# Optimization experiments

Measured on AMD Instinct MI355X. Metric: run time of the kernel, lower is better.

The kernel has to match this reference:

```python
import jax, jax.numpy as jnp
import numpy as np

N_EMBD = 1024
N_HEAD = 16
HEAD_DIM = N_EMBD // N_HEAD


def setup_inputs() -> dict:
    key = jax.random.key(0)
    ks = jax.random.split(key, 5)
    B, T, C = 2, 2048, N_EMBD
    scale = 0.02
    return {
        "x": jax.random.normal(ks[0], (B, T, C), dtype=jnp.float32),
        "w_attn": jax.random.normal(ks[1], (C, 3 * C), dtype=jnp.float32) * scale,
        "b_attn": jax.random.normal(ks[2], (3 * C,), dtype=jnp.float32) * scale,
        "w_proj": jax.random.normal(ks[3], (C, C), dtype=jnp.float32) * scale,
        "b_proj": jax.random.normal(ks[4], (C,), dtype=jnp.float32) * scale,
    }


def reference(x, w_attn, b_attn, w_proj, b_proj):
    B, T, C = x.shape
    H, D = N_HEAD, HEAD_DIM
    qkv = x @ w_attn + b_attn  # [B,T,3C]
    q, k, v = jnp.split(qkv, 3, axis=-1)
    # [B,T,C] -> [B,H,T,D]
    q = q.reshape(B, T, H, D).transpose(0, 2, 1, 3)
    k = k.reshape(B, T, H, D).transpose(0, 2, 1, 3)
    v = v.reshape(B, T, H, D).transpose(0, 2, 1, 3)
    scores = jnp.einsum("bhqd,bhkd->bhqk", q, k) / jnp.sqrt(jnp.float32(D))
    causal = jnp.tril(jnp.ones((T, T), dtype=bool))
    scores = jnp.where(causal, scores, jnp.finfo(scores.dtype).min)
    attn = jax.nn.softmax(scores, axis=-1)
    y = jnp.einsum("bhqk,bhkd->bhqd", attn, v)  # [B,H,T,D]
    y = y.transpose(0, 2, 1, 3).reshape(B, T, C)
    return y @ w_proj + b_proj
```

## Files before the change

kernel.cpp:

```cpp
#include <hip/hip_runtime.h>

typedef unsigned short u16;
typedef u16 u16x4 __attribute__((ext_vector_type(4)));
typedef u16 u16x8 __attribute__((ext_vector_type(8)));
typedef __bf16 bf16x8 __attribute__((ext_vector_type(8)));
typedef float floatx4 __attribute__((ext_vector_type(4)));

#define N_EMBD 1024
#define N_HEAD 16
#define HEAD_DIM 64
#define SEQ 2048
#define BATCH 2
#define M_ROWS (BATCH * SEQ)

typedef __attribute__((address_space(1))) const unsigned char ga_t;
typedef __attribute__((address_space(3))) unsigned char la_t;

#if __has_builtin(__builtin_amdgcn_exp2f)
#define EXP2(x) __builtin_amdgcn_exp2f(x)
#else
#define EXP2(x) exp2f(x)
#endif

__device__ __forceinline__ u16 cvt_bf16(float f) {
  return __builtin_bit_cast(u16, (__bf16)f);
}

__global__ __launch_bounds__(256) void prep(const float* __restrict__ x,
                                            u16* __restrict__ xb,
                                            const float* __restrict__ wa,
                                            const float* __restrict__ wp,
                                            u16* __restrict__ outa,
                                            u16* __restrict__ outp) {
  const int bid = blockIdx.x;
  if (bid < 2048) {
    const long i = ((long)bid * 256 + threadIdx.x) * 8;
    const float4 f0 = *(const float4*)&x[i];
    const float4 f1 = *(const float4*)&x[i + 4];
    u16x8 p;
    p[0] = cvt_bf16(f0.x); p[1] = cvt_bf16(f0.y);
    p[2] = cvt_bf16(f0.z); p[3] = cvt_bf16(f0.w);
    p[4] = cvt_bf16(f1.x); p[5] = cvt_bf16(f1.y);
    p[6] = cvt_bf16(f1.z); p[7] = cvt_bf16(f1.w);
    *(u16x8*)&xb[i] = p;
    return;
  }
  __shared__ u16 tile[32][33];
  const int t = bid - 2048;
  const int gx = t & 127;
  const int gy = t >> 7;
  const int R = N_EMBD;
  const float* in;
  u16* out;
  int C, bx;
  if (gx < 96) {
    in = wa; out = outa; C = 3 * N_EMBD; bx = gx * 32;
  } else {
    in = wp; out = outp; C = N_EMBD; bx = (gx - 96) * 32;
  }
  const int by = gy * 32;
  const int tx = threadIdx.x & 31;
  const int ty = threadIdx.x >> 5;
#pragma unroll
  for (int j = 0; j < 32; j += 8)
    tile[ty + j][tx] = cvt_bf16(in[(long)(by + ty + j) * C + bx + tx]);
  __syncthreads();
#pragma unroll
  for (int j = 0; j < 32; j += 8)
    out[(long)(bx + ty + j) * R + by + tx] = tile[tx][ty + j];
}

#define GBK 64

__device__ __forceinline__ void stage192(const u16* __restrict__ A,
                                         const u16* __restrict__ Bt, int bm,
                                         int bn, int kt, int tid, u16* as,
                                         u16* bs) {
#pragma unroll
  for (int i = 0; i < 2; ++i) {
    const int p = tid + 512 * i;
    const int row = p >> 3;
    const int sl = (p & 7) ^ (row & 7);
    const int wb = (i * 512 + (tid & 448)) * 8;
    __builtin_amdgcn_global_load_lds(
        (ga_t*)&A[(long)(bm + row) * N_EMBD + kt + sl * 8], (la_t*)&as[wb], 16,
        0, 0);
  }
#pragma unroll
  for (int i = 0; i < 3; ++i) {
    const int p = tid + 512 * i;
    const int row = p >> 3;
    const int sl = (p & 7) ^ (row & 7);
    const int wb = (i * 512 + (tid & 448)) * 8;
    __builtin_amdgcn_global_load_lds(
        (ga_t*)&Bt[(long)(bn + row) * N_EMBD + kt + sl * 8], (la_t*)&bs[wb], 16,
        0, 0);
  }
}

__global__ __launch_bounds__(512, 4) void gemm_qkv(
    const u16* __restrict__ A, const u16* __restrict__ Bt,
    const float* __restrict__ bias, u16* __restrict__ qo, u16* __restrict__ ko,
    u16* __restrict__ vo) {
  extern __shared__ u16 smem[];
  u16* As = smem;
  u16* Bs = smem + 2 * 128 * 64;
  const int tid = threadIdx.x;

  const int nx = gridDim.x;
  const int nwg = nx * gridDim.y;
  int lin = blockIdx.y * nx + blockIdx.x;
  lin = (lin & 7) * (nwg >> 3) + (lin >> 3);
  const int bm = (lin / nx) * 128;
  const int bn = (lin % nx) * 192;

  const int w = tid >> 6;
  const int l = tid & 63;
  const int wm = (w >> 2) * 64;
  const int wn = (w & 3) * 48;
  const int m16 = l & 15;
  const int quad = l >> 4;
  const int rsw = m16 & 7;

  floatx4 acc[4][3];
#pragma unroll
  for (int i = 0; i < 4; ++i)
#pragma unroll
    for (int j = 0; j < 3; ++j) acc[i][j] = (floatx4){0.f, 0.f, 0.f, 0.f};

  stage192(A, Bt, bm, bn, 0, tid, As, Bs);
  stage192(A, Bt, bm, bn, GBK, tid, As + 128 * 64, Bs + 192 * 64);
  asm volatile("s_waitcnt vmcnt(5)" ::: "memory");
  __builtin_amdgcn_s_barrier();

  for (int kt = 0; kt < 16; ++kt) {
    u16* as = As + (kt & 1) * (128 * 64);
    u16* bs = Bs + (kt & 1) * (192 * 64);

    bf16x8 af[4][2], bf[3][2];
#pragma unroll
    for (int i = 0; i < 4; ++i)
#pragma unroll
      for (int kk = 0; kk < 2; ++kk)
        af[i][kk] = __builtin_bit_cast(
            bf16x8, *(const u16x8*)&as[(wm + i * 16 + m16) * 64 +
                                       (((kk * 4 + quad) ^ rsw) * 8)]);
#pragma unroll
    for (int j = 0; j < 3; ++j)
#pragma unroll
      for (int kk = 0; kk < 2; ++kk)
        bf[j][kk] = __builtin_bit_cast(
            bf16x8, *(const u16x8*)&bs[(wn + j * 16 + m16) * 64 +
                                       (((kk * 4 + quad) ^ rsw) * 8)]);
    asm volatile("s_waitcnt lgkmcnt(0)" ::: "memory");
    __builtin_amdgcn_s_barrier();

    if (kt + 2 < 16) {
      stage192(A, Bt, bm, bn, (kt + 2) * GBK, tid, as, bs);
      asm volatile("s_waitcnt vmcnt(5)" ::: "memory");
    } else {
      asm volatile("s_waitcnt vmcnt(0)" ::: "memory");
    }
    __builtin_amdgcn_s_barrier();

    __builtin_amdgcn_s_setprio(1);
#pragma unroll
    for (int kk = 0; kk < 2; ++kk)
#pragma unroll
      for (int i = 0; i < 4; ++i)
#pragma unroll
        for (int j = 0; j < 3; ++j)
          acc[i][j] = __builtin_amdgcn_mfma_f32_16x16x32_bf16(
              af[i][kk], bf[j][kk], acc[i][j], 0, 0, 0);
    __builtin_amdgcn_s_setprio(0);
  }

#pragma unroll
  for (int i = 0; i < 4; ++i) {
#pragma unroll
    for (int j = 0; j < 3; ++j) {
      const int col = bn + wn + j * 16 + m16;
      const float bv = bias[col];
      const int which = col >> 10;
      const int cc = col & 1023;
      const int h = cc >> 6;
      const int dd = cc & 63;
      const int row0 = bm + wm + i * 16 + quad * 4;
      const int b = row0 >> 11;
      const int t0 = row0 & 2047;
      if (which == 2) {
        u16x4 pk;
#pragma unroll
        for (int r = 0; r < 4; ++r) pk[r] = cvt_bf16(acc[i][j][r] + bv);
        *(u16x4*)&vo[(((long)(b * N_HEAD + h)) * HEAD_DIM + dd) * SEQ + t0] =
            pk;
      } else {
        u16* dst = (which == 0) ? qo : ko;
#pragma unroll
        for (int r = 0; r < 4; ++r)
          dst[(((long)(b * N_HEAD + h)) * SEQ + t0 + r) * HEAD_DIM + dd] =
              cvt_bf16(acc[i][j][r] + bv);
      }
    }
  }
}

#define PBK 64

__device__ __forceinline__ void stage_proj(const u16* __restrict__ A,
                                           const u16* __restrict__ Bt, int bm,
                                           int bn, int kt, int tid, u16* as,
                                           u16* bs) {
  const int head = kt >> 6;
#pragma unroll
  for (int i = 0; i < 4; ++i) {
    const int p = tid + 256 * i;
    const int row = p >> 3;
    const int sl = (p & 7) ^ (row & 7);
    const int wb = (i * 256 + (tid & 192)) * 8;
    const int m = bm + row;
    const int b = m >> 11, t = m & 2047;
    __builtin_amdgcn_global_load_lds(
        (ga_t*)&A[(((long)(b * N_HEAD + head)) * SEQ + t) * HEAD_DIM + sl * 8],
        (la_t*)&as[wb], 16, 0, 0);
  }
#pragma unroll
  for (int i = 0; i < 2; ++i) {
    const int p = tid + 256 * i;
    const int row = p >> 3;
    const int sl = (p & 7) ^ (row & 7);
    const int wb = (i * 256 + (tid & 192)) * 8;
    __builtin_amdgcn_global_load_lds(
        (ga_t*)&Bt[(long)(bn + row) * N_EMBD + kt + sl * 8], (la_t*)&bs[wb], 16,
        0, 0);
  }
}

__global__ __launch_bounds__(256) void gemm_proj(const u16* __restrict__ A,
                                                 const u16* __restrict__ Bt,
                                                 const float* __restrict__ bias,
                                                 float* __restrict__ out) {
  __shared__ u16 As[2][128 * 64];
  __shared__ u16 Bs[2][64 * 64];
  const int tid = threadIdx.x;

  const int nx = gridDim.x;
  const int nwg = nx * gridDim.y;
  int lin = blockIdx.y * nx + blockIdx.x;
  lin = (lin & 7) * (nwg >> 3) + (lin >> 3);
  const int bm = (lin / nx) * 128;
  const int bn = (lin % nx) * 64;

  const int w = tid >> 6;
  const int l = tid & 63;
  const int wm = (w >> 1) * 64;
  const int wn = (w & 1) * 32;
  const int m16 = l & 15;
  const int quad = l >> 4;
  const int rsw = m16 & 7;

  floatx4 acc[4][2];
#pragma unroll
  for (int i = 0; i < 4; ++i)
#pragma unroll
    for (int j = 0; j < 2; ++j) acc[i][j] = (floatx4){0.f, 0.f, 0.f, 0.f};

  stage_proj(A, Bt, bm, bn, 0, tid, As[0], Bs[0]);
  stage_proj(A, Bt, bm, bn, PBK, tid, As[1], Bs[1]);
  asm volatile("s_waitcnt vmcnt(6)" ::: "memory");
  __builtin_amdgcn_s_barrier();

  for (int kt = 0; kt < 16; ++kt) {
    u16* as = As[kt & 1];
    u16* bs = Bs[kt & 1];

    bf16x8 af[4][2], bf[2][2];
#pragma unroll
    for (int i = 0; i < 4; ++i)
#pragma unroll
      for (int kk = 0; kk < 2; ++kk)
        af[i][kk] = __builtin_bit_cast(
            bf16x8, *(const u16x8*)&as[(wm + i * 16 + m16) * 64 +
                                       (((kk * 4 + quad) ^ rsw) * 8)]);
#pragma unroll
    for (int j = 0; j < 2; ++j)
#pragma unroll
      for (int kk = 0; kk < 2; ++kk)
        bf[j][kk] = __builtin_bit_cast(
            bf16x8, *(const u16x8*)&bs[(wn + j * 16 + m16) * 64 +
                                       (((kk * 4 + quad) ^ rsw) * 8)]);
    asm volatile("s_waitcnt lgkmcnt(0)" ::: "memory");
    __builtin_amdgcn_s_barrier();

    if (kt + 2 < 16) {
      stage_proj(A, Bt, bm, bn, (kt + 2) * PBK, tid, as, bs);
      asm volatile("s_waitcnt vmcnt(6)" ::: "memory");
    } else {
      asm volatile("s_waitcnt vmcnt(0)" ::: "memory");
    }
    __builtin_amdgcn_s_barrier();

    __builtin_amdgcn_s_setprio(1);
#pragma unroll
    for (int kk = 0; kk < 2; ++kk)
#pragma unroll
      for (int i = 0; i < 4; ++i)
#pragma unroll
        for (int j = 0; j < 2; ++j)
          acc[i][j] = __builtin_amdgcn_mfma_f32_16x16x32_bf16(
              af[i][kk], bf[j][kk], acc[i][j], 0, 0, 0);
    __builtin_amdgcn_s_setprio(0);
  }

#pragma unroll
  for (int i = 0; i < 4; ++i) {
#pragma unroll
    for (int j = 0; j < 2; ++j) {
      const int col = bn + wn + j * 16 + m16;
      const float bv = bias[col];
#pragma unroll
      for (int r = 0; r < 4; ++r) {
        const int row = bm + wm + i * 16 + quad * 4 + r;
        out[(long)row * N_EMBD + col] = acc[i][j][r] + bv;
      }
    }
  }
}

#define BQ 64
#define BKV 64
#define LOG2E 1.44269504f
#define NQT (SEQ / BQ)

__device__ __forceinline__ void stage_kv(const u16* __restrict__ K,
                                         const u16* __restrict__ Vt, long bh,
                                         int kt, int tid, u16* kl, u16* vl) {
#pragma unroll
  for (int i = 0; i < 2; ++i) {
    const int p = tid + 256 * i;
    const int row = p >> 3;
    const int slot = (p & 7) ^ (row & 7);
    const int wb = (i * 256 + (tid & 192)) * 8;
    __builtin_amdgcn_global_load_lds(
        (ga_t*)&K[(bh * SEQ + kt + row) * HEAD_DIM + slot * 8], (la_t*)&kl[wb],
        16, 0, 0);
    __builtin_amdgcn_global_load_lds(
        (ga_t*)&Vt[(bh * HEAD_DIM + row) * SEQ + kt + slot * 8], (la_t*)&vl[wb],
        16, 0, 0);
  }
}

__global__ __launch_bounds__(256, 4) void flash_attn(
    u16* __restrict__ Qy, const u16* __restrict__ K,
    const u16* __restrict__ Vt) {
  const int id = blockIdx.x;
  const int r = id >> 8;
  const int c = id & 255;
  const int g = c >> 5;
  const long bh = c & 31;
  const int iq = (r == 0) ? (31 - g)
               : (r == 1) ? (16 + g)
               : (r == 2) ? (15 - g)
                          : g;
  const int tid = threadIdx.x;
  const int w = tid >> 6;
  const int l = tid & 63;
  const int m16 = l & 15;
  const int quad = l >> 4;

  __shared__ u16 Kl[2][BKV * 64];
  __shared__ u16 Vl[2][64 * BKV];
  __shared__ u16 Pl[4][16 * 64];

  const float SC = 0.125f * LOG2E;
  const int qb = iq * BQ;
  const int ntiles = iq + 1;
  const int qglob = qb + w * 16 + m16;
  const int sw = (m16 & 7) << 3;

  bf16x8 qf[2];
  {
    const u16* qrow = Qy + (bh * SEQ + qglob) * HEAD_DIM;
    qf[0] = __builtin_bit_cast(bf16x8, *(const u16x8*)&qrow[quad * 8]);
    qf[1] = __builtin_bit_cast(bf16x8, *(const u16x8*)&qrow[32 + quad * 8]);
  }

  floatx4 Oacc[4];
#pragma unroll
  for (int t = 0; t < 4; ++t) Oacc[t] = (floatx4){0.f, 0.f, 0.f, 0.f};
  float mrow = -1e30f, lsum = 0.f;

  stage_kv(K, Vt, bh, 0, tid, Kl[0], Vl[0]);
  __syncthreads();

  for (int it = 0; it < ntiles; ++it) {
    const int buf = it & 1;
    const int kt = it * BKV;
    if (it + 1 < ntiles)
      stage_kv(K, Vt, bh, kt + BKV, tid, Kl[buf ^ 1], Vl[buf ^ 1]);

    floatx4 s[4];
#pragma unroll
    for (int j = 0; j < 4; ++j) s[j] = (floatx4){0.f, 0.f, 0.f, 0.f};
    __builtin_amdgcn_s_setprio(1);
#pragma unroll
    for (int j = 0; j < 4; ++j)
#pragma unroll
      for (int kk = 0; kk < 2; ++kk) {
        const bf16x8 kf = __builtin_bit_cast(
            bf16x8, *(const u16x8*)&Kl[buf][(j * 16 + m16) * 64 +
                                            ((kk * 32 + quad * 8) ^ sw)]);
        s[j] = __builtin_amdgcn_mfma_f32_16x16x32_bf16(kf, qf[kk], s[j], 0, 0,
                                                       0);
      }
    __builtin_amdgcn_s_setprio(0);
    if (it == ntiles - 1) {
#pragma unroll
      for (int j = 0; j < 4; ++j) {
        const int key0 = kt + j * 16 + quad * 4;
#pragma unroll
        for (int r = 0; r < 4; ++r)
          if (key0 + r > qglob) s[j][r] = -1e30f;
      }
    }

    float tm = s[0][0];
#pragma unroll
    for (int j = 0; j < 4; ++j)
#pragma unroll
      for (int r = 0; r < 4; ++r)
        if (j + r) tm = fmaxf(tm, s[j][r]);
    tm = fmaxf(tm, __shfl_xor(tm, 16, 64));
    tm = fmaxf(tm, __shfl_xor(tm, 32, 64));
    const float pm = tm * SC;
    if (!__all(pm <= mrow + 4.f)) {
      const float mn = fmaxf(mrow, pm);
      const float al = EXP2(mrow - mn);
      mrow = mn;
      lsum *= al;
#pragma unroll
      for (int t = 0; t < 4; ++t)
#pragma unroll
        for (int r = 0; r < 4; ++r) Oacc[t][r] *= al;
    }

    float ls = 0.f;
#pragma unroll
    for (int j = 0; j < 4; ++j) {
      u16x4 pk;
#pragma unroll
      for (int r = 0; r < 4; ++r) {
        const float p = EXP2(__builtin_fmaf(s[j][r], SC, -mrow));
        ls += p;
        pk[r] = cvt_bf16(p);
      }
      *(u16x4*)&Pl[w][m16 * 64 + ((j * 16 + quad * 4) ^ sw)] = pk;
    }
    lsum += ls;

    bf16x8 pf[2];
    pf[0] = __builtin_bit_cast(
        bf16x8, *(const u16x8*)&Pl[w][m16 * 64 + ((quad * 8) ^ sw)]);
    pf[1] = __builtin_bit_cast(
        bf16x8, *(const u16x8*)&Pl[w][m16 * 64 + ((32 + quad * 8) ^ sw)]);
    __builtin_amdgcn_s_setprio(1);
#pragma unroll
    for (int t = 0; t < 4; ++t)
#pragma unroll
      for (int kk = 0; kk < 2; ++kk) {
        const bf16x8 vf = __builtin_bit_cast(
            bf16x8, *(const u16x8*)&Vl[buf][(t * 16 + m16) * 64 +
                                            ((kk * 32 + quad * 8) ^ sw)]);
        Oacc[t] = __builtin_amdgcn_mfma_f32_16x16x32_bf16(vf, pf[kk], Oacc[t],
                                                          0, 0, 0);
      }
    __builtin_amdgcn_s_setprio(0);
    __syncthreads();
  }

  float lt = lsum;
  lt += __shfl_xor(lt, 16, 64);
  lt += __shfl_xor(lt, 32, 64);
  const float invl = 1.f / lt;
#pragma unroll
  for (int t = 0; t < 4; ++t) {
    u16x4 pk;
#pragma unroll
    for (int r = 0; r < 4; ++r) pk[r] = cvt_bf16(Oacc[t][r] * invl);
    *(u16x4*)&Qy[(bh * SEQ + qglob) * HEAD_DIM + t * 16 + quad * 4] = pk;
  }
}

extern "C" void kernel_launch(void* const* d_in, const int* in_sizes, int n_in,
                              void* d_out, int out_size, void* d_ws,
                              size_t ws_size, hipStream_t stream) {
  const float* x = (const float*)d_in[0];
  const float* w_attn = (const float*)d_in[1];
  const float* b_attn = (const float*)d_in[2];
  const float* w_proj = (const float*)d_in[3];
  const float* b_proj = (const float*)d_in[4];
  float* out = (float*)d_out;

  char* ws = (char*)d_ws;
  const size_t SZ = (size_t)BATCH * N_HEAD * SEQ * HEAD_DIM * sizeof(u16);
  u16* q = (u16*)(ws);
  u16* k = (u16*)(ws + SZ);
  u16* vT = (u16*)(ws + 2 * SZ);
  u16* wT_a = (u16*)(ws + 3 * SZ);
  u16* wT_p = (u16*)(ws + 3 * SZ + (size_t)3 * N_EMBD * N_EMBD * sizeof(u16));
  u16* xb = (u16*)(ws + 3 * SZ + (size_t)4 * N_EMBD * N_EMBD * sizeof(u16));

  prep<<<2048 + 4096, 256, 0, stream>>>(x, xb, w_attn, w_proj, wT_a, wT_p);

  gemm_qkv<<<dim3(3 * N_EMBD / 192, M_ROWS / 128), 512,
             (2 * 128 * 64 + 2 * 192 * 64) * sizeof(u16), stream>>>(
      xb, wT_a, b_attn, q, k, vT);

  flash_attn<<<NQT * 32, 256, 0, stream>>>(q, k, vT);

  gemm_proj<<<dim3(N_EMBD / 64, M_ROWS / 128), 256, 0, stream>>>(
      q, wT_p, b_proj, out);
}
```

Baseline: 171.0 us.

## Switch flash attention to 32x32x16 MFMA with register-shuffled P operand

Rewrites the attention inner loop to use 32x32x16 bf16 MFMA tiles, so each wave owns 32 query rows and the block shrinks to two waves (128 threads). The softmax probabilities are repacked into the B-operand layout through cross-half lane shuffles instead of a round trip through the per-wave LDS P buffer. K and V fragments are preloaded into registers ahead of the MFMAs. This removes LDS traffic and row-reduction shuffles, but fewer waves per block and larger accumulators raise register pressure and may reduce latency hiding.

Result: slower. 184.4 us (+7.8%).

```diff
diff --git a/kernel.cpp b/kernel.cpp
--- a/kernel.cpp
+++ b/kernel.cpp
@@ -1,10 +1,13 @@
 #include <hip/hip_runtime.h>
 
 typedef unsigned short u16;
+typedef unsigned int u32;
 typedef u16 u16x4 __attribute__((ext_vector_type(4)));
 typedef u16 u16x8 __attribute__((ext_vector_type(8)));
+typedef u32 u32x4 __attribute__((ext_vector_type(4)));
 typedef __bf16 bf16x8 __attribute__((ext_vector_type(8)));
 typedef float floatx4 __attribute__((ext_vector_type(4)));
+typedef float floatx16 __attribute__((ext_vector_type(16)));
 
 #define N_EMBD 1024
 #define N_HEAD 16
@@ -24,6 +27,9 @@
 
 __device__ __forceinline__ u16 cvt_bf16(float f) {
   return __builtin_bit_cast(u16, (__bf16)f);
+}
+__device__ __forceinline__ u32 pk2(float a, float b) {
+  return (u32)cvt_bf16(a) | ((u32)cvt_bf16(b) << 16);
 }
 
 __global__ __launch_bounds__(256) void prep(const float* __restrict__ x,
@@ -336,11 +342,11 @@
                                          const u16* __restrict__ Vt, long bh,
                                          int kt, int tid, u16* kl, u16* vl) {
 #pragma unroll
-  for (int i = 0; i < 2; ++i) {
-    const int p = tid + 256 * i;
+  for (int i = 0; i < 4; ++i) {
+    const int p = tid + 128 * i;
     const int row = p >> 3;
     const int slot = (p & 7) ^ (row & 7);
-    const int wb = (i * 256 + (tid & 192)) * 8;
+    const int wb = (i * 128 + (tid & 64)) * 8;
     __builtin_amdgcn_global_load_lds(
         (ga_t*)&K[(bh * SEQ + kt + row) * HEAD_DIM + slot * 8], (la_t*)&kl[wb],
         16, 0, 0);
@@ -350,7 +356,7 @@
   }
 }
 
-__global__ __launch_bounds__(256, 4) void flash_attn(
+__global__ __launch_bounds__(128, 2) void flash_attn(
     u16* __restrict__ Qy, const u16* __restrict__ K,
     const u16* __restrict__ Vt) {
   const int id = blockIdx.x;
@@ -365,29 +371,31 @@
   const int tid = threadIdx.x;
   const int w = tid >> 6;
   const int l = tid & 63;
-  const int m16 = l & 15;
-  const int quad = l >> 4;
+  const int q32 = l & 31;
+  const int h = l >> 5;
+  const int l7 = l & 7;
 
   __shared__ u16 Kl[2][BKV * 64];
   __shared__ u16 Vl[2][64 * BKV];
-  __shared__ u16 Pl[4][16 * 64];
 
   const float SC = 0.125f * LOG2E;
   const int qb = iq * BQ;
   const int ntiles = iq + 1;
-  const int qglob = qb + w * 16 + m16;
-  const int sw = (m16 & 7) << 3;
-
-  bf16x8 qf[2];
+  const int qglob = qb + w * 32 + q32;
+
+  bf16x8 qf[4];
   {
     const u16* qrow = Qy + (bh * SEQ + qglob) * HEAD_DIM;
-    qf[0] = __builtin_bit_cast(bf16x8, *(const u16x8*)&qrow[quad * 8]);
-    qf[1] = __builtin_bit_cast(bf16x8, *(const u16x8*)&qrow[32 + quad * 8]);
-  }
-
-  floatx4 Oacc[4];
-#pragma unroll
-  for (int t = 0; t < 4; ++t) Oacc[t] = (floatx4){0.f, 0.f, 0.f, 0.f};
+#pragma unroll
+    for (int ds = 0; ds < 4; ++ds)
+      qf[ds] = __builtin_bit_cast(bf16x8, *(const u16x8*)&qrow[ds * 16 + h * 8]);
+  }
+
+  floatx16 Oacc[2];
+#pragma unroll
+  for (int t = 0; t < 2; ++t)
+#pragma unroll
+    for (int e = 0; e < 16; ++e) Oacc[t][e] = 0.f;
   float mrow = -1e30f, lsum = 0.f;
 
   stage_kv(K, Vt, bh, 0, tid, Kl[0], Vl[0]);
@@ -399,38 +407,57 @@
     if (it + 1 < ntiles)
       stage_kv(K, Vt, bh, kt + BKV, tid, Kl[buf ^ 1], Vl[buf ^ 1]);
 
-    floatx4 s[4];
-#pragma unroll
-    for (int j = 0; j < 4; ++j) s[j] = (floatx4){0.f, 0.f, 0.f, 0.f};
+    bf16x8 kf[2][4];
+#pragma unroll
+    for (int kh = 0; kh < 2; ++kh) {
+      const int krow = kh * 32 + q32;
+#pragma unroll
+      for (int ds = 0; ds < 4; ++ds)
+        kf[kh][ds] = __builtin_bit_cast(
+            bf16x8,
+            *(const u16x8*)&Kl[buf][krow * 64 + (((ds * 2 + h) ^ l7) * 8)]);
+    }
+    floatx16 s[2];
+#pragma unroll
+    for (int kh = 0; kh < 2; ++kh)
+#pragma unroll
+      for (int e = 0; e < 16; ++e) s[kh][e] = 0.f;
     __builtin_amdgcn_s_setprio(1);
 #pragma unroll
-    for (int j = 0; j < 4; ++j)
-#pragma unroll
-      for (int kk = 0; kk < 2; ++kk) {
-        const bf16x8 kf = __builtin_bit_cast(
-            bf16x8, *(const u16x8*)&Kl[buf][(j * 16 + m16) * 64 +
-                                            ((kk * 32 + quad * 8) ^ sw)]);
-        s[j] = __builtin_amdgcn_mfma_f32_16x16x32_bf16(kf, qf[kk], s[j], 0, 0,
-                                                       0);
-      }
+    for (int ds = 0; ds < 4; ++ds)
+#pragma unroll
+      for (int kh = 0; kh < 2; ++kh)
+        s[kh] = __builtin_amdgcn_mfma_f32_32x32x16_bf16(kf[kh][ds], qf[ds],
+                                                        s[kh], 0, 0, 0);
     __builtin_amdgcn_s_setprio(0);
+
+    bf16x8 vf[2][4];
+#pragma unroll
+    for (int dh = 0; dh < 2; ++dh) {
+      const int vrow = dh * 32 + q32;
+#pragma unroll
+      for (int ks = 0; ks < 4; ++ks)
+        vf[dh][ks] = __builtin_bit_cast(
+            bf16x8,
+            *(const u16x8*)&Vl[buf][vrow * 64 + (((ks * 2 + h) ^ l7) * 8)]);
+    }
+
     if (it == ntiles - 1) {
 #pragma unroll
-      for (int j = 0; j < 4; ++j) {
-        const int key0 = kt + j * 16 + quad * 4;
-#pragma unroll
-        for (int r = 0; r < 4; ++r)
-          if (key0 + r > qglob) s[j][r] = -1e30f;
-      }
+      for (int kh = 0; kh < 2; ++kh)
+#pragma unroll
+        for (int reg = 0; reg < 16; ++reg) {
+          const int key = kt + kh * 32 + (reg & 3) + 8 * (reg >> 2) + 4 * h;
+          if (key > qglob) s[kh][reg] = -1e30f;
+        }
     }
 
     float tm = s[0][0];
 #pragma unroll
-    for (int j = 0; j < 4; ++j)
-#pragma unroll
-      for (int r = 0; r < 4; ++r)
-        if (j + r) tm = fmaxf(tm, s[j][r]);
-    tm = fmaxf(tm, __shfl_xor(tm, 16, 64));
+    for (int kh = 0; kh < 2; ++kh)
+#pragma unroll
+      for (int reg = 0; reg < 16; ++reg)
+        if (kh + reg) tm = fmaxf(tm, s[kh][reg]);
     tm = fmaxf(tm, __shfl_xor(tm, 32, 64));
     const float pm = tm * SC;
     if (!__all(pm <= mrow + 4.f)) {
@@ -439,56 +466,65 @@
       mrow = mn;
       lsum *= al;
 #pragma unroll
-      for (int t = 0; t < 4; ++t)
-#pragma unroll
-        for (int r = 0; r < 4; ++r) Oacc[t][r] *= al;
-    }
-
+      for (int t = 0; t < 2; ++t)
+#pragma unroll
+        for (int e = 0; e < 16; ++e) Oacc[t][e] *= al;
+    }
+
+    u32 pr0[2][4], pr1[2][4];
     float ls = 0.f;
 #pragma unroll
-    for (int j = 0; j < 4; ++j) {
-      u16x4 pk;
-#pragma unroll
-      for (int r = 0; r < 4; ++r) {
-        const float p = EXP2(__builtin_fmaf(s[j][r], SC, -mrow));
-        ls += p;
-        pk[r] = cvt_bf16(p);
+    for (int kh = 0; kh < 2; ++kh)
+#pragma unroll
+      for (int m = 0; m < 4; ++m) {
+        const float p0 = EXP2(__builtin_fmaf(s[kh][4 * m + 0], SC, -mrow));
+        const float p1 = EXP2(__builtin_fmaf(s[kh][4 * m + 1], SC, -mrow));
+        const float p2 = EXP2(__builtin_fmaf(s[kh][4 * m + 2], SC, -mrow));
+        const float p3 = EXP2(__builtin_fmaf(s[kh][4 * m + 3], SC, -mrow));
+        ls += (p0 + p1) + (p2 + p3);
+        pr0[kh][m] = pk2(p0, p1);
+        pr1[kh][m] = pk2(p2, p3);
       }
-      *(u16x4*)&Pl[w][m16 * 64 + ((j * 16 + quad * 4) ^ sw)] = pk;
-    }
     lsum += ls;
 
-    bf16x8 pf[2];
-    pf[0] = __builtin_bit_cast(
-        bf16x8, *(const u16x8*)&Pl[w][m16 * 64 + ((quad * 8) ^ sw)]);
-    pf[1] = __builtin_bit_cast(
-        bf16x8, *(const u16x8*)&Pl[w][m16 * 64 + ((32 + quad * 8) ^ sw)]);
     __builtin_amdgcn_s_setprio(1);
 #pragma unroll
-    for (int t = 0; t < 4; ++t)
-#pragma unroll
-      for (int kk = 0; kk < 2; ++kk) {
-        const bf16x8 vf = __builtin_bit_cast(
-            bf16x8, *(const u16x8*)&Vl[buf][(t * 16 + m16) * 64 +
-                                            ((kk * 32 + quad * 8) ^ sw)]);
-        Oacc[t] = __builtin_amdgcn_mfma_f32_16x16x32_bf16(vf, pf[kk], Oacc[t],
-                                                          0, 0, 0);
-      }
+    for (int ks = 0; ks < 4; ++ks) {
+      const int kh = ks >> 1, k2 = ks & 1;
+      const u32 snd0 = h ? pr0[kh][2 * k2] : pr0[kh][2 * k2 + 1];
+      const u32 snd1 = h ? pr1[kh][2 * k2] : pr1[kh][2 * k2 + 1];
+      const u32 rc0 = (u32)__shfl_xor((int)snd0, 32, 64);
+      const u32 rc1 = (u32)__shfl_xor((int)snd1, 32, 64);
+      const u32 ow0 = h ? pr0[kh][2 * k2 + 1] : pr0[kh][2 * k2];
+      const u32 ow1 = h ? pr1[kh][2 * k2 + 1] : pr1[kh][2 * k2];
+      u32x4 fr;
+      fr[0] = h ? rc0 : ow0;
+      fr[1] = h ? rc1 : ow1;
+      fr[2] = h ? ow0 : rc0;
+      fr[3] = h ? ow1 : rc1;
+      const bf16x8 pb = __builtin_bit_cast(bf16x8, fr);
+      Oacc[0] = __builtin_amdgcn_mfma_f32_32x32x16_bf16(vf[0][ks], pb, Oacc[0],
+                                                        0, 0, 0);
+      Oacc[1] = __builtin_amdgcn_mfma_f32_32x32x16_bf16(vf[1][ks], pb, Oacc[1],
+                                                        0, 0, 0);
+    }
     __builtin_amdgcn_s_setprio(0);
     __syncthreads();
   }
 
-  float lt = lsum;
-  lt += __shfl_xor(lt, 16, 64);
-  lt += __shfl_xor(lt, 32, 64);
+  const float lt = lsum + __shfl_xor(lsum, 32, 64);
   const float invl = 1.f / lt;
 #pragma unroll
-  for (int t = 0; t < 4; ++t) {
-    u16x4 pk;
-#pragma unroll
-    for (int r = 0; r < 4; ++r) pk[r] = cvt_bf16(Oacc[t][r] * invl);
-    *(u16x4*)&Qy[(bh * SEQ + qglob) * HEAD_DIM + t * 16 + quad * 4] = pk;
-  }
+  for (int dh = 0; dh < 2; ++dh)
+#pragma unroll
+    for (int rg = 0; rg < 4; ++rg) {
+      u16x4 pk;
+#pragma unroll
+      for (int cc = 0; cc < 4; ++cc)
+        pk[cc] = cvt_bf16(Oacc[dh][rg * 4 + cc] * invl);
+      *(u16x4*)&Qy[(bh * SEQ + qglob) * HEAD_DIM + dh * 32 + rg * 8 + 4 * h] =
+          pk;
+    }
 }
 
 extern "C" void kernel_launch(void* const* d_in, const int* in_sizes, int n_in,
@@ -516,7 +552,7 @@
              (2 * 128 * 64 + 2 * 192 * 64) * sizeof(u16), stream>>>(
       xb, wT_a, b_attn, q, k, vT);
 
-  flash_attn<<<NQT * 32, 256, 0, stream>>>(q, k, vT);
+  flash_attn<<<NQT * 32, 128, 0, stream>>>(q, k, vT);
 
   gemm_proj<<<dim3(N_EMBD / 64, M_ROWS / 128), 256, 0, stream>>>(
       q, wT_p, b_proj, out);
```
